# Kernel tuning notes

Measured on AMD Instinct MI355X. Metric: run time of the kernel, lower is better.

The kernel has to match this reference:

```python
import jax, jax.numpy as jnp
import numpy as np

# --- static CT geometry (shapes must be static under jit; mirrors the `options` vector) ---
B = 8          # batch
V = 720        # number of projection views
D = 736        # detector bins per view
H = 512        # image height (pixels)
W = 512        # image width  (pixels)
DIMG = 0.006641            # image pixel size (physical units)
DDET = 0.0066              # detector bin size
ANG0 = 0.0                 # starting angle
DANG = 2.0 * np.pi / V     # angular step


def setup_inputs() -> dict:
    key = jax.random.key(0)
    proj = jax.random.normal(key, (B, 1, V, D), dtype=jnp.float32)
    options = jnp.array(
        [V, D, W, H, DIMG, DDET, ANG0, DANG, 5.95, 4.906, 0.0, 2.0],
        dtype=jnp.float32,
    )
    return {"proj": proj, "options": options}


def _backproject(sino):
    """Pixel-driven parallel-beam back-projection of one sinogram [V, D] -> image [H, W]."""
    xs = (jnp.arange(W, dtype=jnp.float32) - (W - 1) / 2.0) * DIMG   # pixel-center x
    ys = ((H - 1) / 2.0 - jnp.arange(H, dtype=jnp.float32)) * DIMG   # pixel-center y
    x = jnp.broadcast_to(xs[None, :], (H, W))
    y = jnp.broadcast_to(ys[:, None], (H, W))
    angles = ANG0 + jnp.arange(V, dtype=jnp.float32) * DANG

    def body(acc, inp):
        ang, row = inp                               # row: [D] detector samples at this view
        t = x * jnp.cos(ang) + y * jnp.sin(ang)      # ray coordinate of each pixel
        u = t / DDET + (D - 1) / 2.0                 # fractional detector index
        u0 = jnp.floor(u)
        w = u - u0
        i0 = u0.astype(jnp.int32)
        i1 = i0 + 1
        v0 = jnp.where((i0 >= 0) & (i0 < D), row[jnp.clip(i0, 0, D - 1)], 0.0)
        v1 = jnp.where((i1 >= 0) & (i1 < D), row[jnp.clip(i1, 0, D - 1)], 0.0)
        return acc + (1.0 - w) * v0 + w * v1, None

    acc, _ = jax.lax.scan(body, jnp.zeros((H, W), jnp.float32), (angles, sino))
    return acc * DANG  # angular integration weight


def reference(proj, options):
    # `options` carries the geometry; its shape-determining entries are baked in statically.
    sino = proj.reshape(B, V, D)
    img = jax.vmap(_backproject)(sino)
    return img.reshape(B, 1, H, W)
```

## Files before the change

### kernel.cpp

```cpp
#include <hip/hip_runtime.h>

#define BATCH 8
#define NVIEW 720
#define NPAIR 360
#define NGRP  180
#define NDET  736
#define IMGH  512
#define IMGW  512

#define DANG_F  ((float)(6.283185307179586 / 720.0))
#define RATIO_F ((float)(0.006641 / 0.0066))
#define UCENTER ((float)((NDET - 1) * 0.5))

#define PADDET 768
#define NITER  90
#define ITER_BYTES 12288
#define WS_BYTES ((size_t)BATCH * NITER * PADDET * 16)

#define SWZ(j) ((j) ^ (((j) >> 3) & 7))

typedef float  v2f __attribute__((ext_vector_type(2)));
typedef __fp16 v2h __attribute__((ext_vector_type(2)));
typedef __fp16 v8h __attribute__((ext_vector_type(8)));

struct alignas(16) E16 { v2h ag, bg, am, bm; };

__device__ __forceinline__ void fuse5(const float* __restrict__ fwd,
                                      const float* __restrict__ rev,
                                      int i, float s[5]) {
    const float4 f4 = *(const float4*)(fwd + i);
    const float  f1 = fwd[i + 4];
    const float4 r4 = *(const float4*)(rev + (732 - i));
    const float  r1 = rev[731 - i];
    s[0] = f4.x + r4.w; s[1] = f4.y + r4.z; s[2] = f4.z + r4.y;
    s[3] = f4.w + r4.x; s[4] = f1 + r1;
}

__global__ __launch_bounds__(192) void prep_kernel(
    const float* __restrict__ proj, E16* __restrict__ ws)
{
    const int t = threadIdx.x;
    if (t >= 184) return;
    const int flat = (int)blockIdx.y * 90 + (int)blockIdx.x;
    const int b = flat & 7;
    const int p = flat >> 3;
    const int g = (p < 89) ? p + 1   : 0;
    const int m = (p < 89) ? 179 - p : 90;
    const int i = 4 * t;
    const float* __restrict__ base = proj + (size_t)b * NVIEW * NDET;
    float sAg[5], sBg[5], sAm[5], sBm[5];
    fuse5(base + (size_t)g * NDET,         base + (size_t)(g + 360) * NDET, i, sAg);
    fuse5(base + (size_t)(g + 180) * NDET, base + (size_t)(g + 540) * NDET, i, sBg);
    fuse5(base + (size_t)m * NDET,         base + (size_t)(m + 360) * NDET, i, sAm);
    fuse5(base + (size_t)(m + 180) * NDET, base + (size_t)(m + 540) * NDET, i, sBm);
    E16* __restrict__ dstb = ws + ((size_t)b * NITER + p) * PADDET;
#pragma unroll
    for (int k = 0; k < 4; ++k) {
        E16 e;
        e.ag = __builtin_amdgcn_cvt_pkrtz(sAg[k + 1] - sAg[k], sAg[k]);
        e.bg = __builtin_amdgcn_cvt_pkrtz(sBg[k + 1] - sBg[k], sBg[k]);
        e.am = __builtin_amdgcn_cvt_pkrtz(sAm[k + 1] - sAm[k], sAm[k]);
        e.bm = __builtin_amdgcn_cvt_pkrtz(sBm[k + 1] - sBm[k], sBm[k]);
        const int j = i + k;
        dstb[SWZ(j)] = e;
    }
}

#define VIS(Lp, u, r0, r1, r2, r3) do {                                      \
    const float uu_ = (u);                                                   \
    const int   ii_ = (int)uu_;                                              \
    const v2h wv_ = __builtin_amdgcn_cvt_pkrtz(                              \
        __builtin_amdgcn_fractf(uu_), 1.0f);                                 \
    const v8h E_ = (Lp)[SWZ(ii_)];                                           \
    r0 = __builtin_amdgcn_fdot2((v2h){E_[0], E_[1]}, wv_, r0, false);        \
    r1 = __builtin_amdgcn_fdot2((v2h){E_[2], E_[3]}, wv_, r1, false);        \
    r2 = __builtin_amdgcn_fdot2((v2h){E_[4], E_[5]}, wv_, r2, false);        \
    r3 = __builtin_amdgcn_fdot2((v2h){E_[6], E_[7]}, wv_, r3, false);        \
} while (0)

#define VIS2(Lp, O, u, p0, p1, q0, q1) do {                                  \
    const float uu_ = (u);                                                   \
    const int   ii_ = (int)uu_;                                              \
    const v2h wv_ = __builtin_amdgcn_cvt_pkrtz(                              \
        __builtin_amdgcn_fractf(uu_), 1.0f);                                 \
    const v8h E_ = (Lp)[SWZ(ii_)];                                           \
    const v2h ha_ = {E_[(O)], E_[(O) + 1]};                                  \
    const v2h hb_ = {E_[(O) + 2], E_[(O) + 3]};                              \
    p0 = __builtin_amdgcn_fdot2(ha_, wv_, p0, false);                        \
    p1 = __builtin_amdgcn_fdot2(ha_, wv_, p1, false);                        \
    q0 = __builtin_amdgcn_fdot2(hb_, wv_, q0, false);                        \
    q1 = __builtin_amdgcn_fdot2(hb_, wv_, q1, false);                        \
} while (0)

#define VIS1(Lp, O, u, p0, q0) do {                                          \
    const float uu_ = (u);                                                   \
    const int   ii_ = (int)uu_;                                              \
    const v2h wv_ = __builtin_amdgcn_cvt_pkrtz(                              \
        __builtin_amdgcn_fractf(uu_), 1.0f);                                 \
    const v8h E_ = (Lp)[SWZ(ii_)];                                           \
    p0 = __builtin_amdgcn_fdot2((v2h){E_[(O)], E_[(O) + 1]}, wv_, p0, false);\
    q0 = __builtin_amdgcn_fdot2((v2h){E_[(O) + 2], E_[(O) + 3]}, wv_, q0,    \
                                false);                                      \
} while (0)

__global__ __launch_bounds__(512, 4) void backproject_dma_kernel(
    const v8h* __restrict__ ws, float* __restrict__ out)
{
    __shared__ alignas(16) v8h lds4[4][PADDET];
    __shared__ v2f cs[NGRP];

    const int tid  = threadIdx.x;
    const int wave = tid >> 6;
    const int lane = tid & 63;

    if (tid < NGRP) {
        float s, c;
        sincosf((float)tid * DANG_F, &s, &c);
        cs[tid] = (v2f){c * RATIO_F, s * RATIO_F};
    }

    const int flat = ((int)blockIdx.z * 32 + (int)blockIdx.y) * 2
                     + (int)blockIdx.x;
    const int b    = flat & 7;
    const int tile = flat >> 3;
    const int h = (tile >> 1) * 8 + wave;
    const int w = (tile & 1) * 64 + lane;

    const bool dg = (w == h);
    const bool rm = (w > h);
    const int  H  = rm ? 255 - h : h;
    const int  W  = rm ? 255 - w : w;

    const float px  = (float)W - 255.5f;
    const float py  = 255.5f - (float)H;
    const float px2 = dg ? (-0.5f - (float)W) : py;
    const float py2 = dg ? ( 0.5f + (float)H) : px;

    const char* __restrict__ wsb =
        (const char*)(ws + (size_t)b * NITER * PADDET);

    float A0 = 0.f, A1 = 0.f, A2 = 0.f, A3 = 0.f;
    float B0 = 0.f, B1 = 0.f, B2 = 0.f, B3 = 0.f;
    float X0 = 0.f, X1 = 0.f, X2 = 0.f, X3 = 0.f;
    float Y0 = 0.f, Y1 = 0.f, Y2 = 0.f, Y3 = 0.f;

    auto issue = [&](int p) {
        const char* g0 = wsb + (size_t)p * ITER_BYTES;
        char* l0 = (char*)&lds4[p & 3][0];
        __builtin_amdgcn_global_load_lds(
            (const __attribute__((address_space(1))) void*)
                (g0 + wave * 1024 + lane * 16),
            (__attribute__((address_space(3))) void*)(l0 + wave * 1024),
            16, 0, 0);
        if (wave < 4) {
            const int s = 8 + wave;
            __builtin_amdgcn_global_load_lds(
                (const __attribute__((address_space(1))) void*)
                    (g0 + s * 1024 + lane * 16),
                (__attribute__((address_space(3))) void*)(l0 + s * 1024),
                16, 0, 0);
        }
    };

    const v2f cc = {UCENTER, UCENTER};
    auto groups = [&](int p) {
        const v8h* __restrict__ L = &lds4[p & 3][0];
        const v2f t  = cs[p + 1];
        const v2f m1 = {t.x, -t.y};
        const v2f m2 = {t.y, t.x};
        const v2f gA = __builtin_elementwise_fma(
            (v2f){px, px}, m1, (v2f){py, py} * m2);
        const v2f gB = __builtin_elementwise_fma(
            (v2f){px2, px2}, m1, (v2f){py2, py2} * m2);
        const v2f upA = cc + gA, umA = cc - gA;
        const v2f upB = cc + gB, umB = cc - gB;
        VIS(L, upA.x, A0, A1, X2, X3);
        VIS(L, umA.x, A2, A3, X0, X1);
        VIS(L, upA.y, A3, A0, X3, X0);
        VIS(L, umA.y, A1, A2, X1, X2);
        VIS(L, upB.x, B2, B3, Y0, Y1);
        VIS(L, umB.x, B0, B1, Y2, Y3);
        VIS(L, upB.y, B1, B2, Y1, Y2);
        VIS(L, umB.y, B3, B0, Y3, Y0);
    };

    issue(0);
    issue(1);
    __syncthreads();

    for (int k = 0; k < 44; ++k) {
        issue(2 * k + 2);
        issue(2 * k + 3);
        groups(2 * k);
        groups(2 * k + 1);
        __syncthreads();
    }
    groups(88);

    {
        const v8h* __restrict__ L = &lds4[1][0];
        const v2f t0 = cs[0], t45 = cs[90];
        if (!dg) {
            const float g1 = px * t0.x + py * t0.y;
            const float g2 = -px * t0.y + py * t0.x;
            VIS2(L, 0, UCENTER + g1, A0, X1, A1, X2);
            VIS2(L, 0, UCENTER - g1, A2, X3, A3, X0);
            VIS2(L, 0, UCENTER + g2, A3, X2, A0, X3);
            VIS2(L, 0, UCENTER - g2, A1, X0, A2, X1);
            const float h1 = px * t45.x + py * t45.y;
            const float h2 = -px * t45.y + py * t45.x;
            VIS2(L, 4, UCENTER + h1, A0, X2, A1, X3);
            VIS2(L, 4, UCENTER - h1, A2, X0, A3, X1);
            VIS2(L, 4, UCENTER + h2, A3, X3, A0, X0);
            VIS2(L, 4, UCENTER - h2, A1, X1, A2, X2);
        } else {
            const float g1  = px * t0.x + py * t0.y;
            const float g1b = px2 * t0.x + py2 * t0.y;
            VIS2(L, 0, UCENTER + g1,  A0, A1, A1, A2);
            VIS2(L, 0, UCENTER - g1,  A2, A3, A0, A3);
            VIS2(L, 0, UCENTER + g1b, B2, B3, B3, B0);
            VIS2(L, 0, UCENTER - g1b, B0, B1, B2, B1);
            {
                const v2h wv_ = __builtin_amdgcn_cvt_pkrtz(0.5f, 1.0f);
                const v8h E_ = L[SWZ(367)];
                const v2h ha_ = {E_[4], E_[5]};
                const v2h hb_ = {E_[6], E_[7]};
                A0 = __builtin_amdgcn_fdot2(ha_, wv_, A0, false);
                A2 = __builtin_amdgcn_fdot2(ha_, wv_, A2, false);
                B2 = __builtin_amdgcn_fdot2(ha_, wv_, B2, false);
                B0 = __builtin_amdgcn_fdot2(ha_, wv_, B0, false);
                A1 = __builtin_amdgcn_fdot2(hb_, wv_, A1, false);
                A3 = __builtin_amdgcn_fdot2(hb_, wv_, A3, false);
                B3 = __builtin_amdgcn_fdot2(hb_, wv_, B3, false);
                B1 = __builtin_amdgcn_fdot2(hb_, wv_, B1, false);
            }
            const float e1 = (px + px) * t45.x;
            const float e2 = (px2 + px2) * t45.x;
            VIS1(L, 4, UCENTER + e1, A1, A2);
            VIS1(L, 4, UCENTER - e1, A3, A0);
            VIS1(L, 4, UCENTER + e2, B3, B0);
            VIS1(L, 4, UCENTER - e2, B1, B2);
        }
    }

    const float aE0 = dg ? X0 : Y0, aE1 = dg ? X1 : Y1;
    const float aE2 = dg ? X2 : Y2, aE3 = dg ? X3 : Y3;
    const float bE0 = dg ? Y0 : X0, bE1 = dg ? Y1 : X1;
    const float bE2 = dg ? Y2 : X2, bE3 = dg ? Y3 : X3;
    const float a0 = (A0 + aE0) * DANG_F, a1 = (A1 + aE1) * DANG_F;
    const float a2 = (A2 + aE2) * DANG_F, a3 = (A3 + aE3) * DANG_F;
    const float b0 = (B0 + bE0) * DANG_F, b1 = (B1 + bE1) * DANG_F;
    const float b2 = (B2 + bE2) * DANG_F, b3 = (B3 + bE3) * DANG_F;

    float* __restrict__ o = out + (size_t)b * IMGH * IMGW;
    const int Qr = dg ? 256 + H : W;
    const int Qc = dg ? 256 + W : H;
    o[H * IMGW + W]                         = a0;
    o[(511 - W) * IMGW + H]                 = a1;
    o[(511 - H) * IMGW + (511 - W)]         = a2;
    o[W * IMGW + (511 - H)]                 = a3;
    o[Qr * IMGW + Qc]                       = b0;
    o[(511 - Qc) * IMGW + Qr]               = b1;
    o[(511 - Qr) * IMGW + (511 - Qc)]       = b2;
    o[Qc * IMGW + (511 - Qr)]               = b3;
}

struct Stage { float4 f4, r4; float f1, r1; };

__device__ __forceinline__ void fb_load(const float* __restrict__ sino,
                                        int k, int t, Stage& S) {
    if (t < 368) {
        const int p  = (t >= 184);
        const int i  = 4 * (t - 184 * p);
        const int vf = k + 180 * p;
        const float* __restrict__ fwd = sino + vf * NDET;
        const float* __restrict__ rev = sino + (vf + NPAIR) * NDET;
        S.f4 = *(const float4*)(fwd + i);
        S.f1 = fwd[i + 4];
        S.r4 = *(const float4*)(rev + (732 - i));
        S.r1 = rev[731 - i];
    }
}

__device__ __forceinline__ void fb_write(v2h* __restrict__ L, int t,
                                         const Stage& S) {
    if (t < 368) {
        const int p = (t >= 184);
        const int i = 4 * (t - 184 * p);
        const float s0 = S.f4.x + S.r4.w;
        const float s1 = S.f4.y + S.r4.z;
        const float s2 = S.f4.z + S.r4.y;
        const float s3 = S.f4.w + S.r4.x;
        const float s4 = S.f1 + S.r1;
        const v2h n0 = __builtin_amdgcn_cvt_pkrtz(s1 - s0, s0);
        const v2h n1 = __builtin_amdgcn_cvt_pkrtz(s2 - s1, s1);
        const v2h n2 = __builtin_amdgcn_cvt_pkrtz(s3 - s2, s2);
        const v2h n3 = __builtin_amdgcn_cvt_pkrtz(s4 - s3, s3);
        struct alignas(16) H4 { v2h a, b, c, d; };
        *(H4*)(L + p * NDET + i) = H4{n0, n1, n2, n3};
    }
}

__device__ __forceinline__ void fb_visit(const v2h* __restrict__ L,
                                         float u, float& accA, float& accB) {
    const int   i0 = (int)u;
    const float fr = __builtin_amdgcn_fractf(u);
    const v2h wv = __builtin_amdgcn_cvt_pkrtz(fr, 1.0f);
    const v2h A = L[i0];
    const v2h B = L[i0 + NDET];
    accA = __builtin_amdgcn_fdot2(A, wv, accA, false);
    accB = __builtin_amdgcn_fdot2(B, wv, accB, false);
}

__global__ __launch_bounds__(512, 4) void backproject_fb_kernel(
    const float* __restrict__ proj, float* __restrict__ out)
{
    __shared__ alignas(16) v2h lds[2][2][2 * NDET];
    __shared__ v2f cs[NGRP];

    const int tid = threadIdx.x;
    if (tid < NGRP) {
        float s, c;
        sincosf((float)tid * DANG_F, &s, &c);
        cs[tid] = (v2f){c * RATIO_F, s * RATIO_F};
    }

    const int b    = blockIdx.z;
    const int lane = tid & 63;
    const int h    = (int)blockIdx.y * 8 + (tid >> 6);
    const int w0   = (int)blockIdx.x * 64 + lane;

    const float px = (float)w0 - (float)(IMGW - 1) * 0.5f;
    const float py = (float)(IMGH - 1) * 0.5f - (float)h;

    const float* __restrict__ sino = proj + (size_t)b * NVIEW * NDET;

    float a0 = 0.f, a1 = 0.f, a2 = 0.f, a3 = 0.f;
    float b0 = 0.f, b1 = 0.f, b2 = 0.f, b3 = 0.f;

    Stage s0 = {}, s1 = {};
    fb_load(sino, 0, tid, s0);
    fb_load(sino, 1, tid, s1);
    fb_write(lds[0][0], tid, s0);
    fb_write(lds[0][1], tid, s1);
    fb_load(sino, 2, tid, s0);
    fb_load(sino, 3, tid, s1);
    __syncthreads();

    for (int gg = 0; gg < NGRP; gg += 2) {
        const int buf = (gg >> 1) & 1;
#pragma unroll
        for (int sub = 0; sub < 2; ++sub) {
            const v2h* __restrict__ L = lds[buf][sub];
            const v2f t = cs[gg + sub];
            const v2f m1 = {t.x, -t.y};
            const v2f m2 = {t.y, t.x};
            const v2f pxv = {px, px};
            const v2f pyv = {py, py};
            const v2f gvec = __builtin_elementwise_fma(pxv, m1, pyv * m2);
            const v2f cc = {UCENTER, UCENTER};
            const v2f up = cc + gvec;
            const v2f um = cc - gvec;
            const v2f dd = {128.0f, 128.0f};
            const v2f dm = dd * m1;
            const v2f vp = up + dm;
            const v2f vm = um - dm;

            fb_visit(L, up.x, a0, a1);
            fb_visit(L, um.x, a2, a3);
            fb_visit(L, up.y, a3, a0);
            fb_visit(L, um.y, a1, a2);
            fb_visit(L, vp.x, b0, b1);
            fb_visit(L, vm.x, b2, b3);
            fb_visit(L, vp.y, b3, b0);
            fb_visit(L, vm.y, b1, b2);
        }
        if (gg < NGRP - 2) {
            fb_write(lds[buf ^ 1][0], tid, s0);
            fb_write(lds[buf ^ 1][1], tid, s1);
            if (gg < NGRP - 4) {
                fb_load(sino, gg + 4, tid, s0);
                fb_load(sino, gg + 5, tid, s1);
            }
            __syncthreads();
        }
    }

    float* __restrict__ o = out + (size_t)b * IMGH * IMGW;
    const int hm  = (IMGH - 1) - h;
    const int w1  = w0 + 128;
    const int wm0 = (IMGW - 1) - w0;
    const int wm1 = (IMGW - 1) - w1;
    o[h   * IMGW + w0 ] = a0 * DANG_F;
    o[wm0 * IMGW + h  ] = a1 * DANG_F;
    o[hm  * IMGW + wm0] = a2 * DANG_F;
    o[w0  * IMGW + hm ] = a3 * DANG_F;
    o[h   * IMGW + w1 ] = b0 * DANG_F;
    o[wm1 * IMGW + h  ] = b1 * DANG_F;
    o[hm  * IMGW + wm1] = b2 * DANG_F;
    o[w1  * IMGW + hm ] = b3 * DANG_F;
}

extern "C" void kernel_launch(void* const* d_in, const int* in_sizes, int n_in,
                              void* d_out, int out_size, void* d_ws, size_t ws_size,
                              hipStream_t stream) {
    const float* proj = (const float*)d_in[0];
    float* out = (float*)d_out;

    if (ws_size >= WS_BYTES) {
        E16* ws = (E16*)d_ws;
        prep_kernel<<<dim3(90, BATCH), 192, 0, stream>>>(proj, ws);
        backproject_dma_kernel<<<dim3(2, 32, BATCH), 512, 0, stream>>>(
            (const v8h*)ws, out);
    } else {
        backproject_fb_kernel<<<dim3(2, 32, BATCH), 512, 0, stream>>>(proj, out);
    }
}
```

Measured before the change: 144.6 us.

## Fuse prep and backprojection into one kernel with a grid-wide atomic barrier

Merges the prep kernel into the backprojection kernel: each of the 512 blocks first builds one or two prep units of the fp16 workspace, then all blocks wait on a global atomic counter before running the backprojection. This removes one kernel launch and the gap between the two kernels, at the cost of a memset and a spin barrier that assumes all 512 blocks are resident at once. It also drops the XOR swizzle on workspace and LDS indices, which makes address math simpler but may bring back LDS bank conflicts.

Result: slower. 360.5 us (+149.4%).

```diff
diff --git a/kernel.cpp b/kernel.cpp
--- a/kernel.cpp
+++ b/kernel.cpp
@@ -15,9 +15,8 @@
 #define PADDET 768
 #define NITER  90
 #define ITER_BYTES 12288
+#define NBLOCKS 512
 #define WS_BYTES ((size_t)BATCH * NITER * PADDET * 16)
-
-#define SWZ(j) ((j) ^ (((j) >> 3) & 7))
 
 typedef float  v2f __attribute__((ext_vector_type(2)));
 typedef __fp16 v2h __attribute__((ext_vector_type(2)));
@@ -36,14 +35,11 @@
     s[3] = f4.w + r4.x; s[4] = f1 + r1;
 }
 
-__global__ __launch_bounds__(192) void prep_kernel(
-    const float* __restrict__ proj, E16* __restrict__ ws)
-{
-    const int t = threadIdx.x;
-    if (t >= 184) return;
-    const int flat = (int)blockIdx.y * 90 + (int)blockIdx.x;
-    const int b = flat & 7;
-    const int p = flat >> 3;
+__device__ __forceinline__ void prep_unit(const float* __restrict__ proj,
+                                          E16* __restrict__ ws,
+                                          int unit, int t) {
+    const int b = unit & 7;
+    const int p = unit >> 3;
     const int g = (p < 89) ? p + 1   : 0;
     const int m = (p < 89) ? 179 - p : 90;
     const int i = 4 * t;
@@ -53,7 +49,7 @@
     fuse5(base + (size_t)(g + 180) * NDET, base + (size_t)(g + 540) * NDET, i, sBg);
     fuse5(base + (size_t)m * NDET,         base + (size_t)(m + 360) * NDET, i, sAm);
     fuse5(base + (size_t)(m + 180) * NDET, base + (size_t)(m + 540) * NDET, i, sBm);
-    E16* __restrict__ dstb = ws + ((size_t)b * NITER + p) * PADDET;
+    E16* __restrict__ dst = ws + ((size_t)b * NITER + p) * PADDET + i;
 #pragma unroll
     for (int k = 0; k < 4; ++k) {
         E16 e;
@@ -61,8 +57,7 @@
         e.bg = __builtin_amdgcn_cvt_pkrtz(sBg[k + 1] - sBg[k], sBg[k]);
         e.am = __builtin_amdgcn_cvt_pkrtz(sAm[k + 1] - sAm[k], sAm[k]);
         e.bm = __builtin_amdgcn_cvt_pkrtz(sBm[k + 1] - sBm[k], sBm[k]);
-        const int j = i + k;
-        dstb[SWZ(j)] = e;
+        dst[k] = e;
     }
 }
 
@@ -71,7 +66,7 @@
     const int   ii_ = (int)uu_;                                              \
     const v2h wv_ = __builtin_amdgcn_cvt_pkrtz(                              \
         __builtin_amdgcn_fractf(uu_), 1.0f);                                 \
-    const v8h E_ = (Lp)[SWZ(ii_)];                                           \
+    const v8h E_ = (Lp)[ii_];                                                \
     r0 = __builtin_amdgcn_fdot2((v2h){E_[0], E_[1]}, wv_, r0, false);        \
     r1 = __builtin_amdgcn_fdot2((v2h){E_[2], E_[3]}, wv_, r1, false);        \
     r2 = __builtin_amdgcn_fdot2((v2h){E_[4], E_[5]}, wv_, r2, false);        \
@@ -83,7 +78,7 @@
     const int   ii_ = (int)uu_;                                              \
     const v2h wv_ = __builtin_amdgcn_cvt_pkrtz(                              \
         __builtin_amdgcn_fractf(uu_), 1.0f);                                 \
-    const v8h E_ = (Lp)[SWZ(ii_)];                                           \
+    const v8h E_ = (Lp)[ii_];                                                \
     const v2h ha_ = {E_[(O)], E_[(O) + 1]};                                  \
     const v2h hb_ = {E_[(O) + 2], E_[(O) + 3]};                              \
     p0 = __builtin_amdgcn_fdot2(ha_, wv_, p0, false);                        \
@@ -97,18 +92,16 @@
     const int   ii_ = (int)uu_;                                              \
     const v2h wv_ = __builtin_amdgcn_cvt_pkrtz(                              \
         __builtin_amdgcn_fractf(uu_), 1.0f);                                 \
-    const v8h E_ = (Lp)[SWZ(ii_)];                                           \
+    const v8h E_ = (Lp)[ii_];                                                \
     p0 = __builtin_amdgcn_fdot2((v2h){E_[(O)], E_[(O) + 1]}, wv_, p0, false);\
     q0 = __builtin_amdgcn_fdot2((v2h){E_[(O) + 2], E_[(O) + 3]}, wv_, q0,    \
                                 false);                                      \
 } while (0)
 
-__global__ __launch_bounds__(512, 4) void backproject_dma_kernel(
-    const v8h* __restrict__ ws, float* __restrict__ out)
+__device__ __forceinline__ void bp_compute(
+    const v8h* __restrict__ ws, float* __restrict__ out, int flat,
+    v8h (*__restrict__ lds4)[PADDET], v2f* __restrict__ cs)
 {
-    __shared__ alignas(16) v8h lds4[4][PADDET];
-    __shared__ v2f cs[NGRP];
-
     const int tid  = threadIdx.x;
     const int wave = tid >> 6;
     const int lane = tid & 63;
@@ -119,8 +112,6 @@
         cs[tid] = (v2f){c * RATIO_F, s * RATIO_F};
     }
 
-    const int flat = ((int)blockIdx.z * 32 + (int)blockIdx.y) * 2
-                     + (int)blockIdx.x;
     const int b    = flat & 7;
     const int tile = flat >> 3;
     const int h = (tile >> 1) * 8 + wave;
@@ -222,7 +213,7 @@
             VIS2(L, 0, UCENTER - g1b, B0, B1, B2, B1);
             {
                 const v2h wv_ = __builtin_amdgcn_cvt_pkrtz(0.5f, 1.0f);
-                const v8h E_ = L[SWZ(367)];
+                const v8h E_ = L[367];
                 const v2h ha_ = {E_[4], E_[5]};
                 const v2h hb_ = {E_[6], E_[7]};
                 A0 = __builtin_amdgcn_fdot2(ha_, wv_, A0, false);
@@ -265,6 +256,58 @@
     o[Qc * IMGW + (511 - Qr)]               = b3;
 }
 
+__global__ __launch_bounds__(512, 4) void fused_kernel(
+    const float* __restrict__ proj, E16* __restrict__ ws,
+    float* __restrict__ out, unsigned int* __restrict__ ctr)
+{
+    __shared__ alignas(16) v8h lds4[4][PADDET];
+    __shared__ v2f cs[NGRP];
+
+    const int tid  = threadIdx.x;
+    const int flat = ((int)blockIdx.z * 32 + (int)blockIdx.y) * 2
+                     + (int)blockIdx.x;
+
+    if (tid < 368) {
+        const int second = (tid >= 184);
+        const int unit = flat + (second ? NBLOCKS : 0);
+        if (unit < 720)
+            prep_unit(proj, ws, unit, tid - 184 * second);
+    }
+
+    __threadfence();
+    __syncthreads();
+    if (tid == 0) {
+        __hip_atomic_fetch_add(ctr, 1u, __ATOMIC_ACQ_REL,
+                               __HIP_MEMORY_SCOPE_AGENT);
+        while (__hip_atomic_load(ctr, __ATOMIC_ACQUIRE,
+                                 __HIP_MEMORY_SCOPE_AGENT) < NBLOCKS)
+            __builtin_amdgcn_s_sleep(8);
+    }
+    __syncthreads();
+    __threadfence();
+
+    bp_compute((const v8h*)ws, out, flat, lds4, cs);
+}
+
+__global__ __launch_bounds__(192) void prep_kernel(
+    const float* __restrict__ proj, E16* __restrict__ ws)
+{
+    const int t = threadIdx.x;
+    if (t >= 184) return;
+    const int flat = (int)blockIdx.y * 90 + (int)blockIdx.x;
+    prep_unit(proj, ws, flat, t);
+}
+
+__global__ __launch_bounds__(512, 4) void backproject_dma_kernel(
+    const v8h* __restrict__ ws, float* __restrict__ out)
+{
+    __shared__ alignas(16) v8h lds4[4][PADDET];
+    __shared__ v2f cs[NGRP];
+    const int flat = ((int)blockIdx.z * 32 + (int)blockIdx.y) * 2
+                     + (int)blockIdx.x;
+    bp_compute(ws, out, flat, lds4, cs);
+}
+
 struct Stage { float4 f4, r4; float f1, r1; };
 
 __device__ __forceinline__ void fb_load(const float* __restrict__ sino,
@@ -407,7 +450,12 @@
     const float* proj = (const float*)d_in[0];
     float* out = (float*)d_out;
 
-    if (ws_size >= WS_BYTES) {
+    if (ws_size >= WS_BYTES + 64) {
+        E16* ws = (E16*)d_ws;
+        unsigned int* ctr = (unsigned int*)((char*)d_ws + WS_BYTES);
+        hipMemsetAsync(ctr, 0, sizeof(unsigned int), stream);
+        fused_kernel<<<dim3(2, 32, BATCH), 512, 0, stream>>>(proj, ws, out, ctr);
+    } else if (ws_size >= WS_BYTES) {
         E16* ws = (E16*)d_ws;
         prep_kernel<<<dim3(90, BATCH), 192, 0, stream>>>(proj, ws);
         backproject_dma_kernel<<<dim3(2, 32, BATCH), 512, 0, stream>>>(
```
